# Optimization experiments

Measured on AMD Instinct MI355X. Metric: run time of the kernel, lower is better.

Reference implementation:

```python
import jax, jax.numpy as jnp
import numpy as np

B, S, DIN, E, H, L, F, DOUT = 16, 1024, 64, 512, 8, 6, 2048, 2
DH = E // H
EPS = 1e-5

def _make_pe(n, d):
    # replicates PositionalEncoding buffer: pe[pos, 2i]=sin, pe[pos,2i+1]=cos
    pos = np.arange(n, dtype=np.float32)[:, None]
    div = np.exp(np.arange(0, d, 2, dtype=np.float32) * (-np.log(10000.0) / d))
    pe = np.zeros((n, d), dtype=np.float32)
    pe[:, 0::2] = np.sin(pos * div)
    pe[:, 1::2] = np.cos(pos * div)
    return pe

def _layernorm(x, g, b):
    m = jnp.mean(x, axis=-1, keepdims=True)
    v = jnp.mean((x - m) ** 2, axis=-1, keepdims=True)
    return (x - m) * jax.lax.rsqrt(v + EPS) * g + b

def setup_inputs() -> dict:
    key = jax.random.key(0)
    ks = iter(jax.random.split(key, 40))
    def xavier(k, shape):
        fan_in, fan_out = shape[-2], shape[-1]
        lim = np.sqrt(6.0 / (fan_in + fan_out)).astype(np.float32)
        return jax.random.uniform(k, shape, jnp.float32, -lim, lim)
    inp = {}
    inp['x'] = jax.random.normal(next(ks), (B, S, DIN), jnp.float32)
    inp['Win'] = xavier(next(ks), (DIN, E)); inp['b_in'] = jnp.zeros((E,), jnp.float32)
    # pe[:x.size(0)] with batch-first x -> slice first B positions, broadcast over seq
    inp['pe'] = jnp.asarray(_make_pe(B, E))[:, None, :]  # [B,1,E]
    inp['Wq'] = xavier(next(ks), (L, E, E)); inp['bq'] = jnp.zeros((L, E), jnp.float32)
    inp['Wk'] = xavier(next(ks), (L, E, E)); inp['bk'] = jnp.zeros((L, E), jnp.float32)
    inp['Wv'] = xavier(next(ks), (L, E, E)); inp['bv'] = jnp.zeros((L, E), jnp.float32)
    inp['Wo'] = xavier(next(ks), (L, E, E)); inp['bo'] = jnp.zeros((L, E), jnp.float32)
    inp['g1'] = jnp.ones((L, E), jnp.float32); inp['be1'] = jnp.zeros((L, E), jnp.float32)
    inp['W1'] = xavier(next(ks), (L, E, F)); inp['b1'] = jnp.zeros((L, F), jnp.float32)
    inp['W2'] = xavier(next(ks), (L, F, E)); inp['b2'] = jnp.zeros((L, E), jnp.float32)
    inp['g2'] = jnp.ones((L, E), jnp.float32); inp['be2'] = jnp.zeros((L, E), jnp.float32)
    inp['gf'] = jnp.ones((E,), jnp.float32); inp['bef'] = jnp.zeros((E,), jnp.float32)
    inp['Wout'] = xavier(next(ks), (E, DOUT)); inp['bout'] = jnp.zeros((DOUT,), jnp.float32)
    return inp

def reference(x, Win, b_in, pe, Wq, bq, Wk, bk, Wv, bv, Wo, bo,
              g1, be1, W1, b1, W2, b2, g2, be2, gf, bef, Wout, bout):
    scale = 1.0 / np.sqrt(DH).astype(np.float32)
    h = x @ Win + b_in + pe  # [B,S,E], pe broadcast over seq (replicates source bug)
    for i in range(L):
        resid = h
        q = (h @ Wq[i] + bq[i]).reshape(B, S, H, DH)
        k = (h @ Wk[i] + bk[i]).reshape(B, S, H, DH)
        v = (h @ Wv[i] + bv[i]).reshape(B, S, H, DH)
        scores = jnp.einsum('bqhd,bkhd->bhqk', q, k) * scale
        attn = jax.nn.softmax(scores, axis=-1)
        o = jnp.einsum('bhqk,bkhd->bqhd', attn, v).reshape(B, S, E)
        o = o @ Wo[i] + bo[i]
        a = _layernorm(o + resid, g1[i], be1[i])
        f = jax.nn.relu(a @ W1[i] + b1[i]) @ W2[i] + b2[i]
        h = _layernorm(f + a, g2[i], be2[i])
    out = _layernorm(h, gf, bef) @ Wout + bout
    return out
```

## Files before the change

kernel.cpp:

```cpp
#include <hip/hip_runtime.h>
#include <hip/hip_bf16.h>

typedef __bf16 bf16_t;
typedef __bf16 bf16x8 __attribute__((ext_vector_type(8)));
typedef __bf16 bf16x4 __attribute__((ext_vector_type(4)));
typedef float f32x4 __attribute__((ext_vector_type(4)));

#define B_ 16
#define S_ 1024
#define E_ 512
#define H_ 8
#define DH_ 64
#define L_ 6
#define F_ 2048
#define M_ (B_ * S_)

#define EXP2F(x) __builtin_amdgcn_exp2f(x)

#define GLOAD_LDS16(gsrc, ldst) \
    __builtin_amdgcn_global_load_lds((const __attribute__((address_space(1))) void*)(gsrc), \
                                     (__attribute__((address_space(3))) void*)(ldst), 16, 0, 0)

__global__ void cast_bf16_kernel(const float* __restrict__ src, bf16_t* __restrict__ dst, int n) {
    int i = (blockIdx.x * 256 + threadIdx.x) * 4;
    if (i + 3 < n) {
        f32x4 v = *(const f32x4*)&src[i];
        #pragma unroll
        for (int j = 0; j < 4; ++j) dst[i + j] = (bf16_t)v[j];
    }
}

__global__ void castT_kernel(const float* __restrict__ src, bf16_t* __restrict__ dst,
                             int K, int N, size_t dstZ) {
    __shared__ bf16_t tile[32][33];
    size_t so = (size_t)blockIdx.z * K * N;
    size_t dofs = (size_t)blockIdx.z * dstZ;
    int k0 = blockIdx.y * 32, n0 = blockIdx.x * 32;
    int tx = threadIdx.x, ty = threadIdx.y;
    for (int i = ty; i < 32; i += 8)
        tile[i][tx] = (bf16_t)src[so + (size_t)(k0 + i) * N + n0 + tx];
    __syncthreads();
    for (int i = ty; i < 32; i += 8)
        dst[dofs + (size_t)(n0 + i) * K + k0 + tx] = tile[tx][i];
}

__global__ void pack_bias_kernel(const float* __restrict__ bq, const float* __restrict__ bk,
                                 const float* __restrict__ bv, float* __restrict__ dst) {
    int i = blockIdx.x * 256 + threadIdx.x;
    if (i >= L_ * 1536) return;
    int l = i / 1536, c = i % 1536;
    float v = (c < 512) ? bq[l * 512 + c] : (c < 1024 ? bk[l * 512 + c - 512] : bv[l * 512 + c - 1024]);
    dst[i] = v;
}

template<int EPI, bool RELU>
__launch_bounds__(256, 2)
__global__ void gemm_kernel(const bf16_t* __restrict__ A, const bf16_t* __restrict__ BT,
                            const float* __restrict__ bias, bf16_t* __restrict__ out16,
                            const float* __restrict__ auxf, const bf16_t* __restrict__ auxb,
                            bf16_t* __restrict__ outk, bf16_t* __restrict__ outv,
                            int M, int N, int K)
{
    __shared__ bf16_t As[2][128][32];
    __shared__ bf16_t Bs[2][128][32];
    const int tid = threadIdx.x;
    const int lane = tid & 63;
    const int w = tid >> 6;
    const int wm = w >> 1, wn = w & 1;
    const int m0 = blockIdx.x * 128, n0 = blockIdx.y * 128;
    const int l15 = lane & 15, lg = lane >> 4;

    const int srow = w * 32 + (lane >> 2);
    const int scol = (lane & 3) * 8;
    const bf16_t* Ab = A + (size_t)(m0 + srow) * K + scol;
    const bf16_t* Bb = BT + (size_t)(n0 + srow) * K + scol;

    f32x4 acc[4][4] = {};
    const int nt = K >> 5;

    #define STAGE(buf, t) do { \
        size_t ko_ = (size_t)(t) * 32; \
        _Pragma("unroll") \
        for (int j_ = 0; j_ < 2; ++j_) { \
            GLOAD_LDS16(Ab + (size_t)j_ * 16 * K + ko_, &As[buf][w * 32 + j_ * 16][0]); \
            GLOAD_LDS16(Bb + (size_t)j_ * 16 * K + ko_, &Bs[buf][w * 32 + j_ * 16][0]); \
        } } while (0)

    STAGE(0, 0);
    __syncthreads();
    int cur = 0;
    for (int t = 0; t < nt; ++t) {
        if (t + 1 < nt) STAGE(cur ^ 1, t + 1);
        bf16x8 af[4], bfr[4];
        #pragma unroll
        for (int m = 0; m < 4; ++m) af[m] = *(const bf16x8*)&As[cur][wm * 64 + m * 16 + l15][lg * 8];
        #pragma unroll
        for (int n = 0; n < 4; ++n) bfr[n] = *(const bf16x8*)&Bs[cur][wn * 64 + n * 16 + l15][lg * 8];
        __builtin_amdgcn_s_setprio(1);
        #pragma unroll
        for (int m = 0; m < 4; ++m)
            #pragma unroll
            for (int n = 0; n < 4; ++n)
                acc[m][n] = __builtin_amdgcn_mfma_f32_16x16x32_bf16(af[m], bfr[n], acc[m][n], 0, 0, 0);
        __builtin_amdgcn_s_setprio(0);
        __syncthreads();
        cur ^= 1;
    }
    #undef STAGE

    #pragma unroll
    for (int m = 0; m < 4; ++m) {
        #pragma unroll
        for (int n = 0; n < 4; ++n) {
            int col = n0 + wn * 64 + n * 16 + l15;
            float bv = bias[col];
            if (EPI == 4 && col >= 1024) {
                int row0 = m0 + wm * 64 + m * 16 + lg * 4;
                int b = row0 >> 10, s0 = row0 & 1023;
                int vcol = col - 1024;
                bf16x4 pk;
                #pragma unroll
                for (int r = 0; r < 4; ++r) pk[r] = (bf16_t)(acc[m][n][r] + bv);
                *(bf16x4*)&outv[((size_t)(b * H_ + (vcol >> 6)) * DH_ + (vcol & 63)) * S_ + s0] = pk;
            } else {
                #pragma unroll
                for (int r = 0; r < 4; ++r) {
                    int row = m0 + wm * 64 + m * 16 + lg * 4 + r;
                    float v = acc[m][n][r] + bv;
                    if (EPI == 0) {
                        if (RELU) v = fmaxf(v, 0.f);
                        out16[(size_t)row * N + col] = (bf16_t)v;
                    } else if (EPI == 1) {
                        v += auxf[(size_t)(row >> 10) * E_ + col];
                        out16[(size_t)row * N + col] = (bf16_t)v;
                    } else if (EPI == 2) {
                        v += (float)auxb[(size_t)row * N + col];
                        out16[(size_t)row * N + col] = (bf16_t)v;
                    } else {
                        if (col < 512) out16[(size_t)row * 512 + col] = (bf16_t)v;
                        else           outk[(size_t)row * 512 + (col - 512)] = (bf16_t)v;
                    }
                }
            }
        }
    }
}

__launch_bounds__(256, 3)
__global__ void attn_kernel(const bf16_t* __restrict__ q, const bf16_t* __restrict__ k,
                            const bf16_t* __restrict__ vt, bf16_t* __restrict__ o)
{
    const int id = blockIdx.x;
    const int bh_hi = id & 7;
    const int rest = id >> 3;
    const int qb = rest & 7;
    const int bh = bh_hi * 16 + (rest >> 3);
    const int b = bh >> 3, h = bh & 7;
    const int tid = threadIdx.x, lane = tid & 63, w = tid >> 6;
    const int l15 = lane & 15, lg = lane >> 4;
    const int q0 = qb * 128 + w * 32;

    __shared__ bf16_t Ks[2][64 * 64];
    __shared__ bf16_t Vs[2][64 * 64];
    __shared__ char psh_all[4][4096];
    char* psh = psh_all[w];
    const int swz = (l15 & 7) << 4;

    const bf16_t* kb = k + (size_t)b * S_ * E_ + h * DH_;
    const bf16_t* vb = vt + (size_t)(b * H_ + h) * DH_ * S_;

    const int r8 = lane >> 3, c8 = lane & 7;

    #define STAGE_ATTN(buf, kk0) do { \
        _Pragma("unroll") \
        for (int j_ = 0; j_ < 2; ++j_) { \
            int row_ = w * 16 + j_ * 8 + r8; \
            int ch_ = (c8 ^ (row_ & 7)) * 8; \
            GLOAD_LDS16(kb + (size_t)((kk0) + row_) * E_ + ch_, &Ks[buf][(w * 16 + j_ * 8) * 64]); \
            GLOAD_LDS16(vb + (size_t)row_ * S_ + (kk0) + ch_, &Vs[buf][(w * 16 + j_ * 8) * 64]); \
        } } while (0)

    bf16x8 aq[2][2];
    #pragma unroll
    for (int m = 0; m < 2; ++m) {
        const size_t qoff = (size_t)(b * S_ + q0 + m * 16 + l15) * E_ + h * DH_;
        aq[m][0] = *(const bf16x8*)&q[qoff + lg * 8];
        aq[m][1] = *(const bf16x8*)&q[qoff + 32 + lg * 8];
    }

    float mrow[2] = {-1e30f, -1e30f};
    float lrow[2] = {0.f, 0.f};
    f32x4 accO[2][4] = {};

    const float sc = 0.125f * 1.44269504f;
    const int c0 = (lg ^ (l15 & 7)) * 8;
    const int c1 = c0 ^ 32;

    STAGE_ATTN(0, 0);
    __syncthreads();
    int cur = 0;

    for (int it = 0; it < S_ / 64; ++it) {
        if (it + 1 < S_ / 64) STAGE_ATTN(cur ^ 1, (it + 1) * 64);

        f32x4 sf[2][4];
        #pragma unroll
        for (int n = 0; n < 4; ++n) {
            const int r = n * 16 + l15;
            bf16x8 bk0 = *(const bf16x8*)&Ks[cur][r * 64 + c0];
            bf16x8 bk1 = *(const bf16x8*)&Ks[cur][r * 64 + c1];
            __builtin_amdgcn_s_setprio(1);
            #pragma unroll
            for (int m = 0; m < 2; ++m) {
                f32x4 s = {};
                s = __builtin_amdgcn_mfma_f32_16x16x32_bf16(bk0, aq[m][0], s, 0, 0, 0);
                s = __builtin_amdgcn_mfma_f32_16x16x32_bf16(bk1, aq[m][1], s, 0, 0, 0);
                sf[m][n] = s;
            }
            __builtin_amdgcn_s_setprio(0);
        }

        #pragma unroll
        for (int m = 0; m < 2; ++m) {
            float mx = sf[m][0][0];
            #pragma unroll
            for (int n = 0; n < 4; ++n)
                #pragma unroll
                for (int r = 0; r < 4; ++r) mx = fmaxf(mx, sf[m][n][r]);
            mx = fmaxf(mx, __shfl_xor(mx, 16, 64));
            mx = fmaxf(mx, __shfl_xor(mx, 32, 64));
            float mn = fmaxf(mrow[m], mx);
            float msc = mn * sc;
            float al = EXP2F(mrow[m] * sc - msc);
            float ps = 0.f;
            #pragma unroll
            for (int n = 0; n < 4; ++n) {
                bf16x4 pw;
                #pragma unroll
                for (int r = 0; r < 4; ++r) {
                    float pv = EXP2F(fmaf(sf[m][n][r], sc, -msc));
                    ps += pv;
                    pw[r] = (bf16_t)pv;
                }
                *(bf16x4*)(psh + (m * 16 + l15) * 128 + ((n * 32 + lg * 8) ^ swz)) = pw;
            }
            ps += __shfl_xor(ps, 16, 64);
            ps += __shfl_xor(ps, 32, 64);
            lrow[m] = lrow[m] * al + ps;
            mrow[m] = mn;
            #pragma unroll
            for (int dt = 0; dt < 4; ++dt) accO[m][dt] *= al;
        }
        asm volatile("" ::: "memory");

        bf16x8 pa[2][2];
        #pragma unroll
        for (int m = 0; m < 2; ++m)
            #pragma unroll
            for (int kk = 0; kk < 2; ++kk)
                pa[m][kk] = *(const bf16x8*)(psh + (m * 16 + l15) * 128 + ((kk * 64 + lg * 16) ^ swz));
        bf16x8 vv[4];
        #pragma unroll
        for (int dt = 0; dt < 4; ++dt)
            vv[dt] = *(const bf16x8*)&Vs[cur][(dt * 16 + l15) * 64 + c0];
        __builtin_amdgcn_s_setprio(1);
        #pragma unroll
        for (int dt = 0; dt < 4; ++dt)
            #pragma unroll
            for (int m = 0; m < 2; ++m)
                accO[m][dt] = __builtin_amdgcn_mfma_f32_16x16x32_bf16(vv[dt], pa[m][0], accO[m][dt], 0, 0, 0);
        __builtin_amdgcn_s_setprio(0);
        #pragma unroll
        for (int dt = 0; dt < 4; ++dt)
            vv[dt] = *(const bf16x8*)&Vs[cur][(dt * 16 + l15) * 64 + c1];
        __builtin_amdgcn_s_setprio(1);
        #pragma unroll
        for (int dt = 0; dt < 4; ++dt)
            #pragma unroll
            for (int m = 0; m < 2; ++m)
                accO[m][dt] = __builtin_amdgcn_mfma_f32_16x16x32_bf16(vv[dt], pa[m][1], accO[m][dt], 0, 0, 0);
        __builtin_amdgcn_s_setprio(0);

        __syncthreads();
        cur ^= 1;
    }
    #undef STAGE_ATTN

    #pragma unroll
    for (int m = 0; m < 2; ++m) {
        float rl = 1.f / lrow[m];
        #pragma unroll
        for (int dt = 0; dt < 4; ++dt) {
            bf16x4 ov;
            #pragma unroll
            for (int r = 0; r < 4; ++r) ov[r] = (bf16_t)(accO[m][dt][r] * rl);
            *(bf16x4*)&o[(size_t)(b * S_ + q0 + m * 16 + l15) * E_ + h * DH_ + dt * 16 + lg * 4] = ov;
        }
    }
}

__launch_bounds__(256)
__global__ void ln_kernel(const bf16_t* __restrict__ in, const float* __restrict__ g,
                          const float* __restrict__ be, bf16_t* __restrict__ out)
{
    int row = blockIdx.x * 4 + (threadIdx.x >> 6);
    int lane = threadIdx.x & 63;
    bf16x8 v = *(const bf16x8*)&in[(size_t)row * E_ + lane * 8];
    float x[8];
    #pragma unroll
    for (int j = 0; j < 8; ++j) x[j] = (float)v[j];
    float s = 0.f;
    #pragma unroll
    for (int j = 0; j < 8; ++j) s += x[j];
    #pragma unroll
    for (int off = 32; off >= 1; off >>= 1) s += __shfl_xor(s, off, 64);
    float mean = s * (1.f / E_);
    float vs = 0.f;
    #pragma unroll
    for (int j = 0; j < 8; ++j) { float d = x[j] - mean; vs += d * d; }
    #pragma unroll
    for (int off = 32; off >= 1; off >>= 1) vs += __shfl_xor(vs, off, 64);
    float rstd = rsqrtf(vs * (1.f / E_) + 1e-5f);
    bf16x8 y;
    #pragma unroll
    for (int j = 0; j < 8; ++j) {
        int col = lane * 8 + j;
        y[j] = (bf16_t)((x[j] - mean) * rstd * g[col] + be[col]);
    }
    *(bf16x8*)&out[(size_t)row * E_ + lane * 8] = y;
}

__launch_bounds__(256)
__global__ void final_kernel(const bf16_t* __restrict__ in, const float* __restrict__ g,
                             const float* __restrict__ be, const float* __restrict__ Wout,
                             const float* __restrict__ bout, float* __restrict__ out)
{
    int row = blockIdx.x * 4 + (threadIdx.x >> 6);
    int lane = threadIdx.x & 63;
    bf16x8 v = *(const bf16x8*)&in[(size_t)row * E_ + lane * 8];
    float x[8];
    #pragma unroll
    for (int j = 0; j < 8; ++j) x[j] = (float)v[j];
    float s = 0.f;
    #pragma unroll
    for (int j = 0; j < 8; ++j) s += x[j];
    #pragma unroll
    for (int off = 32; off >= 1; off >>= 1) s += __shfl_xor(s, off, 64);
    float mean = s * (1.f / E_);
    float vs = 0.f;
    #pragma unroll
    for (int j = 0; j < 8; ++j) { float d = x[j] - mean; vs += d * d; }
    #pragma unroll
    for (int off = 32; off >= 1; off >>= 1) vs += __shfl_xor(vs, off, 64);
    float rstd = rsqrtf(vs * (1.f / E_) + 1e-5f);
    float p0 = 0.f, p1 = 0.f;
    #pragma unroll
    for (int j = 0; j < 8; ++j) {
        int col = lane * 8 + j;
        float y = (x[j] - mean) * rstd * g[col] + be[col];
        p0 += y * Wout[col * 2 + 0];
        p1 += y * Wout[col * 2 + 1];
    }
    #pragma unroll
    for (int off = 32; off >= 1; off >>= 1) { p0 += __shfl_xor(p0, off, 64); p1 += __shfl_xor(p1, off, 64); }
    if (lane == 0) {
        out[(size_t)row * 2 + 0] = p0 + bout[0];
        out[(size_t)row * 2 + 1] = p1 + bout[1];
    }
}

extern "C" void kernel_launch(void* const* d_in, const int* in_sizes, int n_in,
                              void* d_out, int out_size, void* d_ws, size_t ws_size,
                              hipStream_t stream)
{
    (void)in_sizes; (void)n_in; (void)out_size;
    const float* x    = (const float*)d_in[0];
    const float* Win  = (const float*)d_in[1];
    const float* b_in = (const float*)d_in[2];
    const float* pe   = (const float*)d_in[3];
    const float* Wq   = (const float*)d_in[4];
    const float* bq   = (const float*)d_in[5];
    const float* Wk   = (const float*)d_in[6];
    const float* bk   = (const float*)d_in[7];
    const float* Wv   = (const float*)d_in[8];
    const float* bv   = (const float*)d_in[9];
    const float* Wo   = (const float*)d_in[10];
    const float* bo   = (const float*)d_in[11];
    const float* g1   = (const float*)d_in[12];
    const float* be1  = (const float*)d_in[13];
    const float* W1   = (const float*)d_in[14];
    const float* b1   = (const float*)d_in[15];
    const float* W2   = (const float*)d_in[16];
    const float* b2   = (const float*)d_in[17];
    const float* g2   = (const float*)d_in[18];
    const float* be2  = (const float*)d_in[19];
    const float* gf   = (const float*)d_in[20];
    const float* bef  = (const float*)d_in[21];
    const float* Wout = (const float*)d_in[22];
    const float* bout = (const float*)d_in[23];

    char* p = (char*)d_ws;
    auto take = [&](size_t bytes) { char* r = p; p += (bytes + 255) & ~(size_t)255; return r; };

    bf16_t* xb    = (bf16_t*)take((size_t)M_ * 64 * 2);
    bf16_t* WinT  = (bf16_t*)take((size_t)E_ * 64 * 2);
    bf16_t* WqkvT = (bf16_t*)take((size_t)L_ * 1536 * E_ * 2);
    bf16_t* WoT   = (bf16_t*)take((size_t)L_ * E_ * E_ * 2);
    bf16_t* W1T   = (bf16_t*)take((size_t)L_ * E_ * F_ * 2);
    bf16_t* W2T   = (bf16_t*)take((size_t)L_ * E_ * F_ * 2);
    float*  bqkv  = (float*)take((size_t)L_ * 1536 * 4);
    bf16_t* hb16  = (bf16_t*)take((size_t)M_ * E_ * 2);
    bf16_t* qb16  = (bf16_t*)take((size_t)M_ * E_ * 2);
    bf16_t* kb16  = (bf16_t*)take((size_t)M_ * E_ * 2);
    bf16_t* vtb   = (bf16_t*)take((size_t)M_ * E_ * 2);
    bf16_t* ob16  = (bf16_t*)take((size_t)M_ * E_ * 2);
    bf16_t* tb16  = (bf16_t*)take((size_t)M_ * E_ * 2);
    bf16_t* ab16  = (bf16_t*)take((size_t)M_ * E_ * 2);
    bf16_t* f1b   = qb16;

    if ((size_t)(p - (char*)d_ws) > ws_size) return;

    cast_bf16_kernel<<<dim3(M_ * 64 / 4 / 256), dim3(256), 0, stream>>>(x, xb, M_ * 64);
    castT_kernel<<<dim3(E_ / 32, 64 / 32, 1), dim3(32, 8), 0, stream>>>(Win, WinT, 64, E_, 0);
    castT_kernel<<<dim3(E_ / 32, E_ / 32, L_), dim3(32, 8), 0, stream>>>(
        Wq, WqkvT + (size_t)0 * E_, E_, E_, (size_t)1536 * E_);
    castT_kernel<<<dim3(E_ / 32, E_ / 32, L_), dim3(32, 8), 0, stream>>>(
        Wk, WqkvT + (size_t)512 * E_, E_, E_, (size_t)1536 * E_);
    castT_kernel<<<dim3(E_ / 32, E_ / 32, L_), dim3(32, 8), 0, stream>>>(
        Wv, WqkvT + (size_t)1024 * E_, E_, E_, (size_t)1536 * E_);
    castT_kernel<<<dim3(E_ / 32, E_ / 32, L_), dim3(32, 8), 0, stream>>>(
        Wo, WoT, E_, E_, (size_t)E_ * E_);
    castT_kernel<<<dim3(F_ / 32, E_ / 32, L_), dim3(32, 8), 0, stream>>>(
        W1, W1T, E_, F_, (size_t)E_ * F_);
    castT_kernel<<<dim3(E_ / 32, F_ / 32, L_), dim3(32, 8), 0, stream>>>(
        W2, W2T, F_, E_, (size_t)E_ * F_);
    pack_bias_kernel<<<dim3((L_ * 1536 + 255) / 256), dim3(256), 0, stream>>>(bq, bk, bv, bqkv);

    gemm_kernel<1, false><<<dim3(M_ / 128, E_ / 128), dim3(256), 0, stream>>>(
        xb, WinT, b_in, hb16, pe, nullptr, nullptr, nullptr, M_, E_, 64);

    for (int i = 0; i < L_; ++i) {
        const bf16_t* WqkvTi = WqkvT + (size_t)i * 1536 * E_;
        const bf16_t* WoTi   = WoT + (size_t)i * E_ * E_;
        const bf16_t* W1Ti   = W1T + (size_t)i * E_ * F_;
        const bf16_t* W2Ti   = W2T + (size_t)i * E_ * F_;

        gemm_kernel<4, false><<<dim3(M_ / 128, 1536 / 128), dim3(256), 0, stream>>>(
            hb16, WqkvTi, bqkv + (size_t)i * 1536, qb16, nullptr, nullptr, kb16, vtb, M_, 1536, E_);
        attn_kernel<<<dim3(1024), dim3(256), 0, stream>>>(qb16, kb16, vtb, ob16);
        gemm_kernel<2, false><<<dim3(M_ / 128, E_ / 128), dim3(256), 0, stream>>>(
            ob16, WoTi, bo + i * E_, tb16, nullptr, hb16, nullptr, nullptr, M_, E_, E_);
        ln_kernel<<<dim3(M_ / 4), dim3(256), 0, stream>>>(tb16, g1 + i * E_, be1 + i * E_, ab16);
        gemm_kernel<0, true><<<dim3(M_ / 128, F_ / 128), dim3(256), 0, stream>>>(
            ab16, W1Ti, b1 + i * F_, f1b, nullptr, nullptr, nullptr, nullptr, M_, F_, E_);
        gemm_kernel<2, false><<<dim3(M_ / 128, E_ / 128), dim3(256), 0, stream>>>(
            f1b, W2Ti, b2 + i * E_, tb16, nullptr, ab16, nullptr, nullptr, M_, E_, F_);
        ln_kernel<<<dim3(M_ / 4), dim3(256), 0, stream>>>(tb16, g2 + i * E_, be2 + i * E_, hb16);
    }

    final_kernel<<<dim3(M_ / 4), dim3(256), 0, stream>>>(hb16, gf, bef, Wout, bout, (float*)d_out);
}
```

Before: 1.393 ms.

## Add 128x256-tile 512-thread GEMM with 4-buffer pipelining and swizzled LDS

Adds a new GEMM kernel that uses 8 waves per block and a 128x256 output tile, so each loaded A tile is reused across twice as many columns. It keeps a 4-deep LDS ring with loads issued two stages ahead, waits with vmcnt instead of a full drain, and needs only one barrier per K-step. It also XOR-swizzles the LDS column layout to reduce bank conflicts. All per-layer GEMMs (QKV, out-proj, FFN1, FFN2) move to the new kernel, while the input projection keeps the old simplified kernel. The risks are higher LDS use (96KB per block) and fewer blocks for the N=512 GEMMs.

After: 1.325 ms. 1.05x faster.

```diff
diff --git a/kernel.cpp b/kernel.cpp
--- a/kernel.cpp
+++ b/kernel.cpp
@@ -57,8 +57,7 @@
 __launch_bounds__(256, 2)
 __global__ void gemm_kernel(const bf16_t* __restrict__ A, const bf16_t* __restrict__ BT,
                             const float* __restrict__ bias, bf16_t* __restrict__ out16,
-                            const float* __restrict__ auxf, const bf16_t* __restrict__ auxb,
-                            bf16_t* __restrict__ outk, bf16_t* __restrict__ outv,
+                            const float* __restrict__ auxf,
                             int M, int N, int K)
 {
     __shared__ bf16_t As[2][128][32];
@@ -114,8 +113,106 @@
         for (int n = 0; n < 4; ++n) {
             int col = n0 + wn * 64 + n * 16 + l15;
             float bv = bias[col];
+            #pragma unroll
+            for (int r = 0; r < 4; ++r) {
+                int row = m0 + wm * 64 + m * 16 + lg * 4 + r;
+                float v = acc[m][n][r] + bv;
+                if (EPI == 1) v += auxf[(size_t)(row >> 10) * E_ + col];
+                if (RELU) v = fmaxf(v, 0.f);
+                out16[(size_t)row * N + col] = (bf16_t)v;
+            }
+        }
+    }
+}
+
+template<int EPI, bool RELU>
+__launch_bounds__(512, 2)
+__global__ void gemm2_kernel(const bf16_t* __restrict__ A, const bf16_t* __restrict__ BT,
+                             const float* __restrict__ bias, bf16_t* __restrict__ out16,
+                             const bf16_t* __restrict__ auxb,
+                             bf16_t* __restrict__ outk, bf16_t* __restrict__ outv,
+                             int M, int N, int K)
+{
+    __shared__ bf16_t AB[4][12288];
+    const int tid = threadIdx.x;
+    const int lane = tid & 63;
+    const int w = tid >> 6;
+    const int wr = w >> 2, wc = w & 3;
+    const int m0 = blockIdx.x * 128, n0 = blockIdx.y * 256;
+    const int l15 = lane & 15, lg = lane >> 4;
+
+    const int srow = w * 16 + (lane >> 2);
+    const int scol = ((lane & 3) ^ ((lane >> 3) & 3)) * 8;
+    const int cswz = (lg ^ ((l15 >> 1) & 3)) * 8;
+    const bf16_t* Ab  = A  + (size_t)(m0 + srow) * K + scol;
+    const bf16_t* Bb0 = BT + (size_t)(n0 + srow) * K + scol;
+    const bf16_t* Bb1 = BT + (size_t)(n0 + 128 + srow) * K + scol;
+
+    f32x4 acc[4][4] = {};
+    const int nt = K >> 5;
+
+    #define STAGE3(kt, buf) do { \
+        size_t ko_ = (size_t)(kt) * 32; \
+        GLOAD_LDS16(Ab  + ko_, &AB[buf][w * 512]); \
+        GLOAD_LDS16(Bb0 + ko_, &AB[buf][4096 + w * 512]); \
+        GLOAD_LDS16(Bb1 + ko_, &AB[buf][8192 + w * 512]); \
+    } while (0)
+
+    STAGE3(0, 0);
+    STAGE3(1, 1);
+    asm volatile("s_waitcnt vmcnt(3)" ::: "memory");
+    __builtin_amdgcn_s_barrier();
+
+    int t = 0;
+    for (; t + 2 < nt; ++t) {
+        const int cur = t & 3;
+        bf16x8 af[4], bf[4];
+        #pragma unroll
+        for (int m = 0; m < 4; ++m)
+            af[m] = *(const bf16x8*)&AB[cur][(wr * 64 + m * 16 + l15) * 32 + cswz];
+        #pragma unroll
+        for (int n = 0; n < 4; ++n)
+            bf[n] = *(const bf16x8*)&AB[cur][4096 + (wc * 64 + n * 16 + l15) * 32 + cswz];
+        STAGE3(t + 2, (t + 2) & 3);
+        asm volatile("s_waitcnt vmcnt(3)" ::: "memory");
+        __builtin_amdgcn_s_barrier();
+        __builtin_amdgcn_s_setprio(1);
+        #pragma unroll
+        for (int m = 0; m < 4; ++m)
+            #pragma unroll
+            for (int n = 0; n < 4; ++n)
+                acc[m][n] = __builtin_amdgcn_mfma_f32_16x16x32_bf16(af[m], bf[n], acc[m][n], 0, 0, 0);
+        __builtin_amdgcn_s_setprio(0);
+    }
+    for (; t < nt; ++t) {
+        const int cur = t & 3;
+        bf16x8 af[4], bf[4];
+        #pragma unroll
+        for (int m = 0; m < 4; ++m)
+            af[m] = *(const bf16x8*)&AB[cur][(wr * 64 + m * 16 + l15) * 32 + cswz];
+        #pragma unroll
+        for (int n = 0; n < 4; ++n)
+            bf[n] = *(const bf16x8*)&AB[cur][4096 + (wc * 64 + n * 16 + l15) * 32 + cswz];
+        asm volatile("s_waitcnt vmcnt(0)" ::: "memory");
+        __builtin_amdgcn_s_barrier();
+        __builtin_amdgcn_s_setprio(1);
+        #pragma unroll
+        for (int m = 0; m < 4; ++m)
+            #pragma unroll
+            for (int n = 0; n < 4; ++n)
+                acc[m][n] = __builtin_amdgcn_mfma_f32_16x16x32_bf16(af[m], bf[n], acc[m][n], 0, 0, 0);
+        __builtin_amdgcn_s_setprio(0);
+    }
+    #undef STAGE3
+
+    #pragma unroll
+    for (int m = 0; m < 4; ++m) {
+        #pragma unroll
+        for (int n = 0; n < 4; ++n) {
+            int col = n0 + wc * 64 + n * 16 + l15;
+            float bv = bias[col];
             if (EPI == 4 && col >= 1024) {
-                int row0 = m0 + wm * 64 + m * 16 + lg * 4;
+                int row0 = m0 + wr * 64 + m * 16 + lg * 4;
                 int b = row0 >> 10, s0 = row0 & 1023;
                 int vcol = col - 1024;
                 bf16x4 pk;
@@ -125,13 +222,10 @@
             } else {
                 #pragma unroll
                 for (int r = 0; r < 4; ++r) {
-                    int row = m0 + wm * 64 + m * 16 + lg * 4 + r;
+                    int row = m0 + wr * 64 + m * 16 + lg * 4 + r;
                     float v = acc[m][n][r] + bv;
                     if (EPI == 0) {
                         if (RELU) v = fmaxf(v, 0.f);
-                        out16[(size_t)row * N + col] = (bf16_t)v;
-                    } else if (EPI == 1) {
-                        v += auxf[(size_t)(row >> 10) * E_ + col];
                         out16[(size_t)row * N + col] = (bf16_t)v;
                     } else if (EPI == 2) {
                         v += (float)auxb[(size_t)row * N + col];
@@ -437,7 +531,7 @@
     pack_bias_kernel<<<dim3((L_ * 1536 + 255) / 256), dim3(256), 0, stream>>>(bq, bk, bv, bqkv);
 
     gemm_kernel<1, false><<<dim3(M_ / 128, E_ / 128), dim3(256), 0, stream>>>(
-        xb, WinT, b_in, hb16, pe, nullptr, nullptr, nullptr, M_, E_, 64);
+        xb, WinT, b_in, hb16, pe, M_, E_, 64);
 
     for (int i = 0; i < L_; ++i) {
         const bf16_t* WqkvTi = WqkvT + (size_t)i * 1536 * E_;
@@ -445,16 +539,16 @@
         const bf16_t* W1Ti   = W1T + (size_t)i * E_ * F_;
         const bf16_t* W2Ti   = W2T + (size_t)i * E_ * F_;
 
-        gemm_kernel<4, false><<<dim3(M_ / 128, 1536 / 128), dim3(256), 0, stream>>>(
-            hb16, WqkvTi, bqkv + (size_t)i * 1536, qb16, nullptr, nullptr, kb16, vtb, M_, 1536, E_);
+        gemm2_kernel<4, false><<<dim3(M_ / 128, 1536 / 256), dim3(512), 0, stream>>>(
+            hb16, WqkvTi, bqkv + (size_t)i * 1536, qb16, nullptr, kb16, vtb, M_, 1536, E_);
         attn_kernel<<<dim3(1024), dim3(256), 0, stream>>>(qb16, kb16, vtb, ob16);
-        gemm_kernel<2, false><<<dim3(M_ / 128, E_ / 128), dim3(256), 0, stream>>>(
-            ob16, WoTi, bo + i * E_, tb16, nullptr, hb16, nullptr, nullptr, M_, E_, E_);
+        gemm2_kernel<2, false><<<dim3(M_ / 128, E_ / 256), dim3(512), 0, stream>>>(
+            ob16, WoTi, bo + i * E_, tb16, hb16, nullptr, nullptr, M_, E_, E_);
         ln_kernel<<<dim3(M_ / 4), dim3(256), 0, stream>>>(tb16, g1 + i * E_, be1 + i * E_, ab16);
-        gemm_kernel<0, true><<<dim3(M_ / 128, F_ / 128), dim3(256), 0, stream>>>(
-            ab16, W1Ti, b1 + i * F_, f1b, nullptr, nullptr, nullptr, nullptr, M_, F_, E_);
-        gemm_kernel<2, false><<<dim3(M_ / 128, E_ / 128), dim3(256), 0, stream>>>(
-            f1b, W2Ti, b2 + i * E_, tb16, nullptr, ab16, nullptr, nullptr, M_, E_, F_);
+        gemm2_kernel<0, true><<<dim3(M_ / 128, F_ / 256), dim3(512), 0, stream>>>(
+            ab16, W1Ti, b1 + i * F_, f1b, nullptr, nullptr, nullptr, M_, F_, E_);
+        gemm2_kernel<2, false><<<dim3(M_ / 128, E_ / 256), dim3(512), 0, stream>>>(
+            f1b, W2Ti, b2 + i * E_, tb16, ab16, nullptr, nullptr, M_, E_, F_);
         ln_kernel<<<dim3(M_ / 4), dim3(256), 0, stream>>>(tb16, g2 + i * E_, be2 + i * E_, hb16);
     }
 
```
